# Kernel optimization log

Hardware: AMD Instinct MI355X
Metric: run time of the kernel (lower is better)

Reference implementation:

```python
import jax, jax.numpy as jnp
import numpy as np
from jax import lax

B, T, J = 32, 256, 24

def _build_adj(n):
    parent = [-1,0,0,0,1,2,3,4,5,6,7,8,9,9,9,12,13,14,16,17,18,19,20,21]
    a = np.eye(n, dtype=np.float32)
    for c in range(min(n, len(parent))):
        p = parent[c]
        if 0 <= p < n:
            a[c, p] = 1.0
            a[p, c] = 1.0
    if n > len(parent):
        for j in range(len(parent), n - 1):
            a[j, j + 1] = 1.0
            a[j + 1, j] = 1.0
    d = np.clip(a.sum(1, keepdims=True), 1.0, None)
    return jnp.asarray(a / d)

ADJ = _build_adj(J)  # [J, J] degree-normalized SMPL adjacency


def _axis_angle_to_rot6d(aa):
    # aa: [..., 3] -> [..., 6] (first two columns of rotation matrix, row-major)
    angle = jnp.linalg.norm(aa, axis=-1)
    axis = aa / (angle[..., None] + 1e-8)
    x, y, z = axis[..., 0], axis[..., 1], axis[..., 2]
    zeros = jnp.zeros_like(x)
    K = jnp.stack([zeros, -z, y, z, zeros, -x, -y, x, zeros], axis=-1)
    K = K.reshape(axis.shape[:-1] + (3, 3))
    eye = jnp.eye(3, dtype=aa.dtype)
    cos = jnp.cos(angle)[..., None, None]
    sin = jnp.sin(angle)[..., None, None]
    outer = axis[..., :, None] * axis[..., None, :]
    rot = cos * eye + (1.0 - cos) * outer + sin * K
    return rot[..., :2].reshape(aa.shape[:-1] + (6,))


def _bn(x, p, eps=1e-5):
    # inference BatchNorm2d; p = stacked [gamma, beta, mean, var], each [C]
    g, b, m, v = p
    s = g / jnp.sqrt(v + eps)
    return x * s[None, :, None, None] + (b - m * s)[None, :, None, None]


def _block(x, gcn_w, gcn_b, bn1, tcn_w, tcn_b, bn2, res_w=None, res_b=None):
    # 1x1 conv (pointwise channel mix)
    y = jnp.einsum('oc,bctj->botj', gcn_w, x) + gcn_b[None, :, None, None]
    # graph aggregation over joints
    y = jnp.einsum('bctj,jk->bctk', y, ADJ)
    y = jax.nn.relu(_bn(y, bn1))
    # temporal conv (3,1), padding (1,0); dropout is identity at inference
    y = lax.conv_general_dilated(y, tcn_w, (1, 1), ((1, 1), (0, 0)),
                                 dimension_numbers=('NCHW', 'OIHW', 'NCHW'))
    y = _bn(y + tcn_b[None, :, None, None], bn2)
    if res_w is None:
        r = x
    else:
        r = jnp.einsum('oc,bctj->botj', res_w, x) + res_b[None, :, None, None]
    return jax.nn.relu(y + r)


def setup_inputs() -> dict:
    key = jax.random.key(0)
    ks = iter(jax.random.split(key, 64))
    def rn(shape, s=0.05):
        return jax.random.normal(next(ks), shape, jnp.float32) * s
    def bnp(c):
        g = jax.random.uniform(next(ks), (c,), jnp.float32) * 0.5 + 0.75
        b = rn((c,), 0.1)
        m = rn((c,), 0.1)
        v = jax.random.uniform(next(ks), (c,), jnp.float32) * 0.5 + 0.5
        return jnp.stack([g, b, m, v])
    return {
        'x': jax.random.normal(next(ks), (B, T, J, 3), jnp.float32),
        'b1_gcn_w': rn((128, 6)), 'b1_gcn_b': rn((128,)), 'b1_bn1': bnp(128),
        'b1_tcn_w': rn((128, 128, 3, 1)), 'b1_tcn_b': rn((128,)), 'b1_bn2': bnp(128),
        'b1_res_w': rn((128, 6)), 'b1_res_b': rn((128,)),
        'b2_gcn_w': rn((128, 128)), 'b2_gcn_b': rn((128,)), 'b2_bn1': bnp(128),
        'b2_tcn_w': rn((128, 128, 3, 1)), 'b2_tcn_b': rn((128,)), 'b2_bn2': bnp(128),
        'b3_gcn_w': rn((256, 128)), 'b3_gcn_b': rn((256,)), 'b3_bn1': bnp(256),
        'b3_tcn_w': rn((256, 256, 3, 1)), 'b3_tcn_b': rn((256,)), 'b3_bn2': bnp(256),
        'b3_res_w': rn((256, 128)), 'b3_res_b': rn((256,)),
        'out_w': rn((512, 256)), 'out_b': rn((512,)),
    }


def reference(x, b1_gcn_w, b1_gcn_b, b1_bn1, b1_tcn_w, b1_tcn_b, b1_bn2, b1_res_w, b1_res_b,
              b2_gcn_w, b2_gcn_b, b2_bn1, b2_tcn_w, b2_tcn_b, b2_bn2,
              b3_gcn_w, b3_gcn_b, b3_bn1, b3_tcn_w, b3_tcn_b, b3_bn2, b3_res_w, b3_res_b,
              out_w, out_b):
    rot6d = _axis_angle_to_rot6d(x)                 # [B,T,J,6]
    f = jnp.transpose(rot6d, (0, 3, 1, 2))          # [B,6,T,J]
    f = _block(f, b1_gcn_w, b1_gcn_b, b1_bn1, b1_tcn_w, b1_tcn_b, b1_bn2, b1_res_w, b1_res_b)
    f = _block(f, b2_gcn_w, b2_gcn_b, b2_bn1, b2_tcn_w, b2_tcn_b, b2_bn2)
    f = _block(f, b3_gcn_w, b3_gcn_b, b3_bn1, b3_tcn_w, b3_tcn_b, b3_bn2, b3_res_w, b3_res_b)
    pooled = f.mean(axis=(2, 3))                    # [B,256]
    mu = pooled @ out_w.T + out_b                   # [B,512]
    return mu
```

## Files before the change

kernel.cpp:

```cpp
#include <hip/hip_runtime.h>
#include <math.h>

#define J_ 24
#define T_ 256
#define B_ 32

typedef short short8v __attribute__((ext_vector_type(8)));
typedef float f32x4  __attribute__((ext_vector_type(4)));

__device__ __forceinline__ short f2bf(float f) {
    unsigned u = __float_as_uint(f);
    u += 0x7fffu + ((u >> 16) & 1u);
    return (short)(u >> 16);
}
__device__ __forceinline__ float bf2f(short s) {
    return __uint_as_float(((unsigned)(unsigned short)s) << 16);
}

__device__ __forceinline__ void gload_lds16(const void* gsrc, void* ldst) {
    __builtin_amdgcn_global_load_lds(
        (const __attribute__((address_space(1))) void*)gsrc,
        (__attribute__((address_space(3))) void*)ldst, 16, 0, 0);
}

__device__ __constant__ int d_parent[24] = {-1,0,0,0,1,2,3,4,5,6,7,8,9,9,9,12,13,14,16,17,18,19,20,21};

__global__ void adj_init_kernel(float* __restrict__ adj_out, short* __restrict__ amix) {
    __shared__ float s_adj[576];
    const int tid = threadIdx.x;
    for (int i = tid; i < 576; i += 256) {
        const int j = i / 24, k = i % 24;
        float a = (j == k || d_parent[k] == j || d_parent[j] == k) ? 1.f : 0.f;
        float d = 0.f;
        for (int kk = 0; kk < 24; ++kk)
            d += (j == kk || d_parent[kk] == j || d_parent[j] == kk) ? 1.f : 0.f;
        const float v = a / fmaxf(d, 1.f);
        s_adj[i] = v;
        adj_out[i] = v;
    }
    __syncthreads();
    if (tid < 24) {
        float cs = 0.f;
        for (int j = 0; j < 24; ++j) cs += s_adj[j*24 + tid];
        adj_out[576 + tid] = cs;
        int n = 0;
        for (int j = 0; j < 24; ++j) {
            const float w = s_adj[j*24 + tid];
            if (w != 0.f && n < 8) {
                adj_out[600 + tid*8 + n] = w;
                adj_out[792 + tid*8 + n] = (float)j;
                ++n;
            }
        }
        for (; n < 8; ++n) { adj_out[600 + tid*8 + n] = 0.f; adj_out[792 + tid*8 + n] = 0.f; }
    }
    __syncthreads();
    for (int i = tid; i < 96*96; i += 256) {
        const int r = i / 96, j = i % 96;
        float v = 0.f;
        if (r / 24 == j / 24) v = s_adj[(j % 24) * 24 + (r % 24)];
        amix[i] = f2bf(v);
    }
}

__global__ __launch_bounds__(256) void prep_kernel(
    const float* __restrict__ w1t, const float* __restrict__ bn1_2,
    const float* __restrict__ w2t, const float* __restrict__ bn2_2,
    const float* __restrict__ w3t, const float* __restrict__ bn3_2,
    const float* __restrict__ g2w, const float* __restrict__ bn2_1,
    const float* __restrict__ g3w, const float* __restrict__ bn3_1,
    const float* __restrict__ r3w,
    const float* __restrict__ g1w, const float* __restrict__ bn1_1,
    const float* __restrict__ r1w,
    short* __restrict__ wt1b, short* __restrict__ wt2b, short* __restrict__ wt3b,
    short* __restrict__ gw2b, short* __restrict__ gw3b, short* __restrict__ rw3b,
    short* __restrict__ gw1b, short* __restrict__ rw1b)
{
    const int i = blockIdx.x * 256 + threadIdx.x;
    if (i < 49152) {
        const int o = i / 384, r = i % 384, dt = r / 128, c = r % 128;
        const float s = bn1_2[o] * rsqrtf(bn1_2[384 + o] + 1e-5f);
        wt1b[i] = f2bf(s * w1t[(o*128 + c)*3 + dt]);
    } else if (i < 98304) {
        const int j = i - 49152;
        const int o = j / 384, r = j % 384, dt = r / 128, c = r % 128;
        const float s = bn2_2[o] * rsqrtf(bn2_2[384 + o] + 1e-5f);
        wt2b[j] = f2bf(s * w2t[(o*128 + c)*3 + dt]);
    } else if (i < 294912) {
        const int j = i - 98304;
        const int o = j / 768, r = j % 768, dt = r / 256, c = r % 256;
        const float s = bn3_2[o] * rsqrtf(bn3_2[768 + o] + 1e-5f);
        wt3b[j] = f2bf(s * w3t[(o*256 + c)*3 + dt]);
    } else if (i < 311296) {
        const int j = i - 294912;
        const int o = j / 128;
        const float s = bn2_1[o] * rsqrtf(bn2_1[384 + o] + 1e-5f);
        gw2b[j] = f2bf(s * g2w[j]);
    } else if (i < 344064) {
        const int j = i - 311296;
        const int o = j / 128;
        const float s = bn3_1[o] * rsqrtf(bn3_1[768 + o] + 1e-5f);
        gw3b[j] = f2bf(s * g3w[j]);
    } else if (i < 376832) {
        const int j = i - 344064;
        rw3b[j] = f2bf(r3w[j]);
    } else if (i < 378880) {
        const int j = i - 376832;
        const int o = j / 8, c = j & 7;
        const float s = bn1_1[o] * rsqrtf(bn1_1[384 + o] + 1e-5f);
        gw1b[j] = (c < 6) ? f2bf(s * g1w[o*6 + c]) : (short)0;
    } else if (i < 380928) {
        const int j = i - 378880;
        const int o = j / 8, c = j & 7;
        rw1b[j] = (c < 6) ? f2bf(r1w[o*6 + c]) : (short)0;
    }
}

#define LDS_SZ   52832
#define FA_OFF   26624
#define FT_STRIDE 208
#define X6B_OFF  40320
#define XA6B_OFF 44928
#define TBL_OFF  51200

__global__ __launch_bounds__(512) void block1_kernel(
    const float* __restrict__ x,
    const short* __restrict__ gw1b, const float* __restrict__ gb1, const float* __restrict__ bn1,
    const short* __restrict__ rw1b, const float* __restrict__ rb1,
    const float* __restrict__ bn12, const float* __restrict__ tb1, const short* __restrict__ wt1b,
    const short* __restrict__ gw2b, const float* __restrict__ gb2, const float* __restrict__ bn21,
    const float* __restrict__ adjp, const short* __restrict__ amix,
    short* __restrict__ f1_out, short* __restrict__ h2_out)
{
    __shared__ char smem[LDS_SZ];
    short* s_x6b  = (short*)(smem + X6B_OFF);
    short* s_xa6b = (short*)(smem + XA6B_OFF);
    float* s_cw  = (float*)(smem + TBL_OFF);
    int*   s_ci  = (int*)  (smem + TBL_OFF + 768);
    float* s_cs  = (float*)(smem + TBL_OFF + 1536);

    const int r0 = blockIdx.x * 96;
    const int bstart = (r0 / 6144) * 6144;
    const int bend = bstart + 6144;
    const int tid = threadIdx.x;
    const int l = tid & 63, wid = tid >> 6;
    const int m0w = (wid >> 2) * 48;
    const int n0w = (wid & 3) * 32;
    const int lr = l & 15, lk = l >> 4;
    const short8v z8 = {0,0,0,0,0,0,0,0};

    if (tid < 192) { s_cw[tid] = adjp[600 + tid]; s_ci[tid] = (int)adjp[792 + tid]; }
    else if (tid < 216) s_cs[tid - 192] = adjp[576 + (tid - 192)];
    if (tid < 144) {
        const int gr = r0 - 24 + tid;
        short8v v = z8;
        if (gr >= bstart && gr < bend) {
            const float ax = x[gr*3+0], ay = x[gr*3+1], az = x[gr*3+2];
            const float angle = sqrtf(ax*ax + ay*ay + az*az);
            const float inv = 1.f / (angle + 1e-8f);
            const float ux = ax*inv, uy = ay*inv, uz = az*inv;
            const float c = cosf(angle), s = sinf(angle), omc = 1.f - c;
            v[0] = f2bf(c + omc*ux*ux);   v[1] = f2bf(omc*ux*uy - s*uz);
            v[2] = f2bf(omc*uy*ux + s*uz); v[3] = f2bf(c + omc*uy*uy);
            v[4] = f2bf(omc*uz*ux - s*uy); v[5] = f2bf(omc*uz*uy + s*ux);
        }
        *(short8v*)(s_x6b + tid*8) = v;
    }
    __syncthreads();
    if (tid < 144) {
        const int k = tid % 24, sl = (tid / 24) * 24;
        float a[6] = {0,0,0,0,0,0};
        #pragma unroll
        for (int u = 0; u < 8; ++u) {
            const float wgt = s_cw[k*8+u];
            const short8v v = *(const short8v*)(s_x6b + (sl + s_ci[k*8+u])*8);
            #pragma unroll
            for (int e = 0; e < 6; ++e) a[e] = fmaf(wgt, bf2f(v[e]), a[e]);
        }
        short8v o8 = z8;
        #pragma unroll
        for (int e = 0; e < 6; ++e) o8[e] = f2bf(a[e]);
        *(short8v*)(s_xa6b + tid*8) = o8;
    }
    __syncthreads();
    {
        const int col = wid*16 + lr;
        short8v bfr = z8;
        if (lk == 0) bfr = *(const short8v*)(gw1b + (size_t)col*8);
        f32x4 cacc[9];
        #pragma unroll
        for (int mi = 0; mi < 9; ++mi) cacc[mi] = (f32x4){0.f,0.f,0.f,0.f};
        #pragma unroll
        for (int mi = 0; mi < 9; ++mi) {
            short8v afr = z8;
            if (lk == 0) afr = *(const short8v*)(s_xa6b + (mi*16 + lr)*8);
            cacc[mi] = __builtin_amdgcn_mfma_f32_16x16x32_bf16(afr, bfr, cacc[mi], 0, 0, 0);
        }
        const float s1 = bn1[col] * rsqrtf(bn1[384 + col] + 1e-5f);
        const float t1 = bn1[128 + col] - bn1[256 + col] * s1;
        const float g1 = s1 * gb1[col];
        const int ch2 = col * 2;
        #pragma unroll
        for (int mi = 0; mi < 9; ++mi)
            #pragma unroll
            for (int rg = 0; rg < 4; ++rg) {
                const int row = mi*16 + lk*4 + rg;
                const int gr = r0 - 24 + row;
                short hv = 0;
                if (gr >= bstart && gr < bend)
                    hv = f2bf(fmaxf(cacc[mi][rg] + t1 + g1*s_cs[row % 24], 0.f));
                *(short*)(smem + row*256 + ((ch2 & 0xF0) ^ ((row&7)<<4)) + (ch2 & 14)) = hv;
            }
    }
    __syncthreads();
    f32x4 acc[3][2];
    #pragma unroll
    for (int mi = 0; mi < 3; ++mi)
        #pragma unroll
        for (int ni = 0; ni < 2; ++ni) acc[mi][ni] = (f32x4){0.f,0.f,0.f,0.f};
    #pragma unroll
    for (int dt = 0; dt < 3; ++dt) {
        #pragma unroll
        for (int kc = 0; kc < 4; ++kc) {
            short8v bfr[2], afr[3];
            #pragma unroll
            for (int ni = 0; ni < 2; ++ni) {
                const int n = n0w + ni*16 + lr;
                bfr[ni] = *(const short8v*)(wt1b + (size_t)n*384 + dt*128 + kc*32 + lk*8);
            }
            #pragma unroll
            for (int mi = 0; mi < 3; ++mi) {
                const int row = m0w + dt*24 + mi*16 + lr;
                afr[mi] = *(const short8v*)(smem + row*256 + ((kc*64 + lk*16) ^ ((row&7)<<4)));
            }
            #pragma unroll
            for (int mi = 0; mi < 3; ++mi)
                #pragma unroll
                for (int ni = 0; ni < 2; ++ni)
                    acc[mi][ni] = __builtin_amdgcn_mfma_f32_16x16x32_bf16(afr[mi], bfr[ni], acc[mi][ni], 0, 0, 0);
        }
    }
    {
        short8v bfr[2], afr[3];
        #pragma unroll
        for (int ni = 0; ni < 2; ++ni) {
            bfr[ni] = z8;
            if (lk == 0) bfr[ni] = *(const short8v*)(rw1b + (size_t)(n0w + ni*16 + lr)*8);
        }
        #pragma unroll
        for (int mi = 0; mi < 3; ++mi) {
            afr[mi] = z8;
            if (lk == 0) afr[mi] = *(const short8v*)(s_x6b + (m0w + mi*16 + lr + 24)*8);
        }
        #pragma unroll
        for (int mi = 0; mi < 3; ++mi)
            #pragma unroll
            for (int ni = 0; ni < 2; ++ni)
                acc[mi][ni] = __builtin_amdgcn_mfma_f32_16x16x32_bf16(afr[mi], bfr[ni], acc[mi][ni], 0, 0, 0);
    }
    __syncthreads();
    #pragma unroll
    for (int ni = 0; ni < 2; ++ni) {
        const int o = n0w + ni*16 + lr;
        const float s2 = bn12[o] * rsqrtf(bn12[384 + o] + 1e-5f);
        const float bias = (bn12[128 + o] - bn12[256 + o]*s2) + s2*tb1[o] + rb1[o];
        #pragma unroll
        for (int mi = 0; mi < 3; ++mi)
            #pragma unroll
            for (int rg = 0; rg < 4; ++rg) {
                const int rl = m0w + mi*16 + lk*4 + rg;
                const short hv = f2bf(fmaxf(acc[mi][ni][rg] + bias, 0.f));
                f1_out[(size_t)(r0 + rl)*128 + o] = hv;
                *(short*)(smem + o*FT_STRIDE + rl*2) = hv;
            }
    }
    __syncthreads();
    {
        f32x4 pacc[3][2];
        #pragma unroll
        for (int mi = 0; mi < 3; ++mi)
            #pragma unroll
            for (int ni = 0; ni < 2; ++ni) pacc[mi][ni] = (f32x4){0.f,0.f,0.f,0.f};
        #pragma unroll
        for (int kc = 0; kc < 3; ++kc) {
            short8v bfr[2], afr[3];
            #pragma unroll
            for (int ni = 0; ni < 2; ++ni) {
                const int ch = n0w + ni*16 + lr;
                bfr[ni] = *(const short8v*)(smem + ch*FT_STRIDE + kc*64 + lk*16);
            }
            #pragma unroll
            for (int mi = 0; mi < 3; ++mi) {
                const int row = m0w + mi*16 + lr;
                afr[mi] = *(const short8v*)(amix + row*96 + kc*32 + lk*8);
            }
            #pragma unroll
            for (int mi = 0; mi < 3; ++mi)
                #pragma unroll
                for (int ni = 0; ni < 2; ++ni)
                    pacc[mi][ni] = __builtin_amdgcn_mfma_f32_16x16x32_bf16(afr[mi], bfr[ni], pacc[mi][ni], 0, 0, 0);
        }
        __syncthreads();
        #pragma unroll
        for (int ni = 0; ni < 2; ++ni) {
            const int ch2 = (n0w + ni*16 + lr) * 2;
            #pragma unroll
            for (int mi = 0; mi < 3; ++mi)
                #pragma unroll
                for (int rg = 0; rg < 4; ++rg) {
                    const int row = m0w + mi*16 + lk*4 + rg;
                    *(short*)(smem + FA_OFF + row*256 + ((ch2 & 0xF0) ^ ((row&7)<<4)) + (ch2 & 14)) =
                        f2bf(pacc[mi][ni][rg]);
                }
        }
    }
    __syncthreads();
    #pragma unroll
    for (int mi = 0; mi < 3; ++mi)
        #pragma unroll
        for (int ni = 0; ni < 2; ++ni) acc[mi][ni] = (f32x4){0.f,0.f,0.f,0.f};
    #pragma unroll
    for (int kc = 0; kc < 4; ++kc) {
        short8v bfr[2], afr[3];
        #pragma unroll
        for (int ni = 0; ni < 2; ++ni) {
            const int n = n0w + ni*16 + lr;
            bfr[ni] = *(const short8v*)(gw2b + (size_t)n*128 + kc*32 + lk*8);
        }
        #pragma unroll
        for (int mi = 0; mi < 3; ++mi) {
            const int row = m0w + mi*16 + lr;
            afr[mi] = *(const short8v*)(smem + FA_OFF + row*256 + ((kc*64 + lk*16) ^ ((row&7)<<4)));
        }
        #pragma unroll
        for (int mi = 0; mi < 3; ++mi)
            #pragma unroll
            for (int ni = 0; ni < 2; ++ni)
                acc[mi][ni] = __builtin_amdgcn_mfma_f32_16x16x32_bf16(afr[mi], bfr[ni], acc[mi][ni], 0, 0, 0);
    }
    #pragma unroll
    for (int ni = 0; ni < 2; ++ni) {
        const int o = n0w + ni*16 + lr;
        const float s = bn21[o] * rsqrtf(bn21[384 + o] + 1e-5f);
        const float t = bn21[128 + o] - bn21[256 + o]*s;
        const float g = s * gb2[o];
        #pragma unroll
        for (int mi = 0; mi < 3; ++mi)
            #pragma unroll
            for (int rg = 0; rg < 4; ++rg) {
                const int rl = m0w + mi*16 + lk*4 + rg;
                h2_out[(size_t)(r0 + rl)*128 + o] = f2bf(fmaxf(acc[mi][ni][rg] + t + g*s_cs[rl % 24], 0.f));
            }
    }
}

__global__ __launch_bounds__(512) void block2_kernel(
    const short* __restrict__ h2, const short* __restrict__ wt2b,
    const float* __restrict__ bn22, const float* __restrict__ tb2,
    const short* __restrict__ f1,
    const short* __restrict__ gw3b, const float* __restrict__ gb3, const float* __restrict__ bn31,
    const float* __restrict__ adjp, const short* __restrict__ amix,
    const char* __restrict__ zbuf,
    short* __restrict__ f2_out, short* __restrict__ h3_out)
{
    __shared__ char smem[LDS_SZ];
    float* s_cs  = (float*)(smem + TBL_OFF + 1536);

    const int r0 = blockIdx.x * 96;
    const int bstart = (r0 / 6144) * 6144;
    const int bend = bstart + 6144;
    const int tid = threadIdx.x;
    const int l = tid & 63, wid = tid >> 6;
    const int m0w = (wid >> 2) * 48;
    const int lr = l & 15, lk = l >> 4;

    if (tid < 24) s_cs[tid] = adjp[576 + tid];
    for (int ck = wid; ck < 36; ck += 8) {
        const int row = ck*4 + (l >> 4);
        const int cg = (l & 15) ^ (row & 7);
        const int gr = r0 - 24 + row;
        const void* gsrc = (gr >= bstart && gr < bend)
            ? (const void*)(h2 + (size_t)gr*128 + cg*8)
            : (const void*)(zbuf + cg*16);
        gload_lds16(gsrc, smem + ck*1024);
    }
    __syncthreads();
    {
        const int n0w = (wid & 3) * 32;
        f32x4 acc[3][2];
        #pragma unroll
        for (int mi = 0; mi < 3; ++mi)
            #pragma unroll
            for (int ni = 0; ni < 2; ++ni) acc[mi][ni] = (f32x4){0.f,0.f,0.f,0.f};
        #pragma unroll
        for (int dt = 0; dt < 3; ++dt) {
            #pragma unroll
            for (int kc = 0; kc < 4; ++kc) {
                short8v bfr[2], afr[3];
                #pragma unroll
                for (int ni = 0; ni < 2; ++ni) {
                    const int n = n0w + ni*16 + lr;
                    bfr[ni] = *(const short8v*)(wt2b + (size_t)n*384 + dt*128 + kc*32 + lk*8);
                }
                #pragma unroll
                for (int mi = 0; mi < 3; ++mi) {
                    const int row = m0w + dt*24 + mi*16 + lr;
                    afr[mi] = *(const short8v*)(smem + row*256 + ((kc*64 + lk*16) ^ ((row&7)<<4)));
                }
                #pragma unroll
                for (int mi = 0; mi < 3; ++mi)
                    #pragma unroll
                    for (int ni = 0; ni < 2; ++ni)
                        acc[mi][ni] = __builtin_amdgcn_mfma_f32_16x16x32_bf16(afr[mi], bfr[ni], acc[mi][ni], 0, 0, 0);
            }
        }
        __syncthreads();
        #pragma unroll
        for (int ni = 0; ni < 2; ++ni) {
            const int o = n0w + ni*16 + lr;
            const float s = bn22[o] * rsqrtf(bn22[384 + o] + 1e-5f);
            const float bias = (bn22[128 + o] - bn22[256 + o]*s) + s*tb2[o];
            #pragma unroll
            for (int mi = 0; mi < 3; ++mi)
                #pragma unroll
                for (int rg = 0; rg < 4; ++rg) {
                    const int rl = m0w + mi*16 + lk*4 + rg;
                    const float res = bf2f(f1[(size_t)(r0 + rl)*128 + o]);
                    const short hv = f2bf(fmaxf(acc[mi][ni][rg] + bias + res, 0.f));
                    *(short*)(smem + o*FT_STRIDE + rl*2) = hv;
                    f2_out[(size_t)(r0 + rl)*128 + o] = hv;
                }
        }
    }
    __syncthreads();
    {
        const int n0w = (wid & 3) * 32;
        f32x4 pacc[3][2];
        #pragma unroll
        for (int mi = 0; mi < 3; ++mi)
            #pragma unroll
            for (int ni = 0; ni < 2; ++ni) pacc[mi][ni] = (f32x4){0.f,0.f,0.f,0.f};
        #pragma unroll
        for (int kc = 0; kc < 3; ++kc) {
            short8v bfr[2], afr[3];
            #pragma unroll
            for (int ni = 0; ni < 2; ++ni) {
                const int ch = n0w + ni*16 + lr;
                bfr[ni] = *(const short8v*)(smem + ch*FT_STRIDE + kc*64 + lk*16);
            }
            #pragma unroll
            for (int mi = 0; mi < 3; ++mi) {
                const int row = m0w + mi*16 + lr;
                afr[mi] = *(const short8v*)(amix + row*96 + kc*32 + lk*8);
            }
            #pragma unroll
            for (int mi = 0; mi < 3; ++mi)
                #pragma unroll
                for (int ni = 0; ni < 2; ++ni)
                    pacc[mi][ni] = __builtin_amdgcn_mfma_f32_16x16x32_bf16(afr[mi], bfr[ni], pacc[mi][ni], 0, 0, 0);
        }
        __syncthreads();
        #pragma unroll
        for (int ni = 0; ni < 2; ++ni) {
            const int ch2 = (n0w + ni*16 + lr) * 2;
            #pragma unroll
            for (int mi = 0; mi < 3; ++mi)
                #pragma unroll
                for (int rg = 0; rg < 4; ++rg) {
                    const int row = m0w + mi*16 + lk*4 + rg;
                    *(short*)(smem + FA_OFF + row*256 + ((ch2 & 0xF0) ^ ((row&7)<<4)) + (ch2 & 14)) =
                        f2bf(pacc[mi][ni][rg]);
                }
        }
    }
    __syncthreads();
    {
        const int n0w = (wid & 3) * 64;
        f32x4 acc[3][4];
        #pragma unroll
        for (int mi = 0; mi < 3; ++mi)
            #pragma unroll
            for (int ni = 0; ni < 4; ++ni) acc[mi][ni] = (f32x4){0.f,0.f,0.f,0.f};
        #pragma unroll
        for (int kc = 0; kc < 4; ++kc) {
            short8v bfr[4], afr[3];
            #pragma unroll
            for (int ni = 0; ni < 4; ++ni) {
                const int n = n0w + ni*16 + lr;
                bfr[ni] = *(const short8v*)(gw3b + (size_t)n*128 + kc*32 + lk*8);
            }
            #pragma unroll
            for (int mi = 0; mi < 3; ++mi) {
                const int row = m0w + mi*16 + lr;
                afr[mi] = *(const short8v*)(smem + FA_OFF + row*256 + ((kc*64 + lk*16) ^ ((row&7)<<4)));
            }
            #pragma unroll
            for (int mi = 0; mi < 3; ++mi)
                #pragma unroll
                for (int ni = 0; ni < 4; ++ni)
                    acc[mi][ni] = __builtin_amdgcn_mfma_f32_16x16x32_bf16(afr[mi], bfr[ni], acc[mi][ni], 0, 0, 0);
        }
        #pragma unroll
        for (int ni = 0; ni < 4; ++ni) {
            const int o = n0w + ni*16 + lr;
            const float s = bn31[o] * rsqrtf(bn31[768 + o] + 1e-5f);
            const float t = bn31[256 + o] - bn31[512 + o]*s;
            const float g = s * gb3[o];
            #pragma unroll
            for (int mi = 0; mi < 3; ++mi)
                #pragma unroll
                for (int rg = 0; rg < 4; ++rg) {
                    const int rl = m0w + mi*16 + lk*4 + rg;
                    h3_out[(size_t)(r0 + rl)*256 + o] = f2bf(fmaxf(acc[mi][ni][rg] + t + g*s_cs[rl % 24], 0.f));
                }
        }
    }
}

__global__ __launch_bounds__(512) void conv3_pool_kernel(
    const short* __restrict__ A, const short* __restrict__ Bw,
    const float* __restrict__ bn, const float* __restrict__ tb,
    const short* __restrict__ f2, const short* __restrict__ rw3b, const float* __restrict__ rb3,
    const char* __restrict__ zbuf, float* __restrict__ pooled)
{
    __shared__ char lds[240 * 256];
    const int cpx = gridDim.x >> 3;
    const int bid = blockIdx.x;
    const int tile = (bid % 8) * cpx + bid / 8;
    const int r0 = tile * 192;
    const int bb = r0 / 6144;
    const int bstart = bb * 6144, bend = bstart + 6144;
    const int tid = threadIdx.x, l = tid & 63, wid = tid >> 6;
    const int m0w = (wid >> 2) * 96;
    const int n0w = (wid & 3) * 64;
    const int lr = l & 15, lk = l >> 4;

    f32x4 acc[6][4];
    #pragma unroll
    for (int mi = 0; mi < 6; ++mi)
        #pragma unroll
        for (int ni = 0; ni < 4; ++ni) acc[mi][ni] = (f32x4){0.f,0.f,0.f,0.f};

    for (int p = 0; p < 2; ++p) {
        if (p) __syncthreads();
        for (int ck = wid; ck < 60; ck += 8) {
            const int row = ck*4 + (l >> 4);
            const int cg = (l & 15) ^ (row & 7);
            const int gr = r0 - 24 + row;
            const void* gsrc = (gr >= bstart && gr < bend)
                ? (const void*)(A + (size_t)gr*256 + p*128 + cg*8)
                : (const void*)(zbuf + cg*16);
            gload_lds16(gsrc, lds + ck*1024);
        }
        __syncthreads();
        #pragma unroll
        for (int dt = 0; dt < 3; ++dt) {
            #pragma unroll
            for (int kc = 0; kc < 4; ++kc) {
                short8v bfr[4], afr[6];
                #pragma unroll
                for (int ni = 0; ni < 4; ++ni) {
                    const int n = n0w + ni * 16 + lr;
                    bfr[ni] = *(const short8v*)(Bw + (size_t)n * 768 + dt * 256 + p * 128 + kc * 32 + lk * 8);
                }
                #pragma unroll
                for (int mi = 0; mi < 6; ++mi) {
                    const int row = m0w + dt * 24 + mi * 16 + lr;
                    afr[mi] = *(const short8v*)(lds + row * 256 + ((kc * 64 + lk * 16) ^ ((row & 7) << 4)));
                }
                #pragma unroll
                for (int mi = 0; mi < 6; ++mi)
                    #pragma unroll
                    for (int ni = 0; ni < 4; ++ni)
                        acc[mi][ni] = __builtin_amdgcn_mfma_f32_16x16x32_bf16(afr[mi], bfr[ni], acc[mi][ni], 0, 0, 0);
            }
        }
    }
    __syncthreads();
    for (int ck = wid; ck < 48; ck += 8) {
        const int row = ck*4 + (l >> 4);
        const int cg = (l & 15) ^ (row & 7);
        gload_lds16((const void*)(f2 + (size_t)(r0 + row)*128 + cg*8), lds + ck*1024);
    }
    __syncthreads();
    #pragma unroll
    for (int kc = 0; kc < 4; ++kc) {
        short8v bfr[4], afr[6];
        #pragma unroll
        for (int ni = 0; ni < 4; ++ni) {
            const int n = n0w + ni * 16 + lr;
            bfr[ni] = *(const short8v*)(rw3b + (size_t)n * 128 + kc * 32 + lk * 8);
        }
        #pragma unroll
        for (int mi = 0; mi < 6; ++mi) {
            const int row = m0w + mi * 16 + lr;
            afr[mi] = *(const short8v*)(lds + row * 256 + ((kc * 64 + lk * 16) ^ ((row & 7) << 4)));
        }
        #pragma unroll
        for (int mi = 0; mi < 6; ++mi)
            #pragma unroll
            for (int ni = 0; ni < 4; ++ni)
                acc[mi][ni] = __builtin_amdgcn_mfma_f32_16x16x32_bf16(afr[mi], bfr[ni], acc[mi][ni], 0, 0, 0);
    }

    float psum[4] = {0.f, 0.f, 0.f, 0.f};
    #pragma unroll
    for (int ni = 0; ni < 4; ++ni) {
        const int o = n0w + ni * 16 + lr;
        const float s = bn[o] * rsqrtf(bn[768 + o] + 1e-5f);
        const float t = bn[256 + o] - bn[512 + o] * s;
        const float bias = s * tb[o] + t + rb3[o];
        #pragma unroll
        for (int mi = 0; mi < 6; ++mi)
            #pragma unroll
            for (int rg = 0; rg < 4; ++rg)
                psum[ni] += fmaxf(acc[mi][ni][rg] + bias, 0.f);
    }
    #pragma unroll
    for (int ni = 0; ni < 4; ++ni) {
        float v = psum[ni];
        v += __shfl_xor(v, 16);
        v += __shfl_xor(v, 32);
        if (l < 16) atomicAdd(pooled + (size_t)bb * 256 + (n0w + ni * 16 + l), v);
    }
}

__global__ __launch_bounds__(256) void head_kernel(const float* __restrict__ pooled_sums,
    const float* __restrict__ ow, const float* __restrict__ ob, float* __restrict__ outp) {
    __shared__ float pooled[256];
    const int b = blockIdx.x, tid = threadIdx.x;
    pooled[tid] = pooled_sums[(size_t)b*256 + tid] * (1.f/6144.f);
    __syncthreads();
    for (int rep = 0; rep < 2; ++rep) {
        const int oo = rep*256 + tid;
        float a = ob[oo];
        const float4* wr = (const float4*)(ow + (size_t)oo*256);
        for (int c4 = 0; c4 < 64; ++c4) {
            const float4 w = wr[c4];
            const float4 p = *(const float4*)&pooled[c4*4];
            a += w.x*p.x + w.y*p.y + w.z*p.z + w.w*p.w;
        }
        outp[(size_t)b*512 + oo] = a;
    }
}

extern "C" void kernel_launch(void* const* d_in, const int* in_sizes, int n_in,
                              void* d_out, int out_size, void* d_ws, size_t ws_size,
                              hipStream_t stream)
{
    const float* x        = (const float*)d_in[0];
    const float* b1_gcn_w = (const float*)d_in[1];
    const float* b1_gcn_b = (const float*)d_in[2];
    const float* b1_bn1   = (const float*)d_in[3];
    const float* b1_tcn_w = (const float*)d_in[4];
    const float* b1_tcn_b = (const float*)d_in[5];
    const float* b1_bn2   = (const float*)d_in[6];
    const float* b1_res_w = (const float*)d_in[7];
    const float* b1_res_b = (const float*)d_in[8];
    const float* b2_gcn_w = (const float*)d_in[9];
    const float* b2_gcn_b = (const float*)d_in[10];
    const float* b2_bn1   = (const float*)d_in[11];
    const float* b2_tcn_w = (const float*)d_in[12];
    const float* b2_tcn_b = (const float*)d_in[13];
    const float* b2_bn2   = (const float*)d_in[14];
    const float* b3_gcn_w = (const float*)d_in[15];
    const float* b3_gcn_b = (const float*)d_in[16];
    const float* b3_bn1   = (const float*)d_in[17];
    const float* b3_tcn_w = (const float*)d_in[18];
    const float* b3_tcn_b = (const float*)d_in[19];
    const float* b3_bn2   = (const float*)d_in[20];
    const float* b3_res_w = (const float*)d_in[21];
    const float* b3_res_b = (const float*)d_in[22];
    const float* out_w    = (const float*)d_in[23];
    const float* out_b    = (const float*)d_in[24];

    char* w = (char*)d_ws;
    float* adjp = (float*)w;   w += 4096;
    short* wt1b = (short*)w;   w += 98304;
    short* wt2b = (short*)w;   w += 98304;
    short* wt3b = (short*)w;   w += 393216;
    short* gw2b = (short*)w;   w += 32768;
    short* gw3b = (short*)w;   w += 65536;
    short* rw3b = (short*)w;   w += 65536;
    short* amixb = (short*)w;  w += 18432;
    short* gw1b = (short*)w;   w += 4096;
    short* rw1b = (short*)w;   w += 4096;
    float* pooled = (float*)w; w += 32768;
    char* zbuf = w;            w += 1024;
    const size_t fixed = (size_t)(w - (char*)d_ws);

    int G = 1;
    {
        const int tiers[6] = {32, 16, 8, 4, 2, 1};
        for (int ti = 0; ti < 6; ++ti) {
            const size_t need = fixed + (size_t)tiers[ti] * 6291456ull;
            if (need <= ws_size) { G = tiers[ti]; break; }
        }
    }
    const size_t MG = (size_t)G * 6144;

    short* f1 = (short*)w;
    short* h2 = f1 + MG*128;
    short* h3 = h2 + MG*128;
    short* f2 = f1;

    hipMemsetAsync(pooled, 0, 32768 + 1024, stream);
    adj_init_kernel<<<1, 256, 0, stream>>>(adjp, amixb);
    prep_kernel<<<1488, 256, 0, stream>>>(b1_tcn_w, b1_bn2, b2_tcn_w, b2_bn2, b3_tcn_w, b3_bn2,
                                          b2_gcn_w, b2_bn1, b3_gcn_w, b3_bn1, b3_res_w,
                                          b1_gcn_w, b1_bn1, b1_res_w,
                                          wt1b, wt2b, wt3b, gw2b, gw3b, rw3b, gw1b, rw1b);

    for (int b0 = 0; b0 < B_; b0 += G) {
        block1_kernel<<<64*G, 512, 0, stream>>>(
            x + (size_t)b0*6144*3,
            gw1b, b1_gcn_b, b1_bn1, rw1b, b1_res_b,
            b1_bn2, b1_tcn_b, wt1b,
            gw2b, b2_gcn_b, b2_bn1, adjp, amixb, f1, h2);
        block2_kernel<<<64*G, 512, 0, stream>>>(
            h2, wt2b, b2_bn2, b2_tcn_b, f1,
            gw3b, b3_gcn_b, b3_bn1, adjp, amixb, zbuf, f2, h3);
        conv3_pool_kernel<<<32*G, 512, 0, stream>>>(
            h3, wt3b, b3_bn2, b3_tcn_b, f2, rw3b, b3_res_b, zbuf, pooled + (size_t)b0*256);
    }

    head_kernel<<<B_, 256, 0, stream>>>(pooled, out_w, out_b, (float*)d_out);
}
```

Measured before the change: 418.5 us.

## Halve conv3 tile rows and double-buffer the K-half loads in conv3_pool

Shrinks each conv3_pool block from 192 to 96 rows and doubles the grid, which gives more blocks for the CUs to schedule. It splits LDS into two buffers so the second K-half of the activation tile and the residual input load while MFMAs run on the first. This cuts accumulator registers and exposed load latency. The cost is that each block now reloads the same weights and halo rows over fewer output rows and issues more atomics into pooled.

```diff
diff --git a/kernel.cpp b/kernel.cpp
--- a/kernel.cpp
+++ b/kernel.cpp
@@ -523,81 +523,111 @@
     const short* __restrict__ f2, const short* __restrict__ rw3b, const float* __restrict__ rb3,
     const char* __restrict__ zbuf, float* __restrict__ pooled)
 {
-    __shared__ char lds[240 * 256];
+    __shared__ char lds[2 * 36864];
+    char* buf0 = lds;
+    char* buf1 = lds + 36864;
     const int cpx = gridDim.x >> 3;
     const int bid = blockIdx.x;
     const int tile = (bid % 8) * cpx + bid / 8;
-    const int r0 = tile * 192;
+    const int r0 = tile * 96;
     const int bb = r0 / 6144;
     const int bstart = bb * 6144, bend = bstart + 6144;
     const int tid = threadIdx.x, l = tid & 63, wid = tid >> 6;
-    const int m0w = (wid >> 2) * 96;
+    const int m0w = (wid >> 2) * 48;
     const int n0w = (wid & 3) * 64;
     const int lr = l & 15, lk = l >> 4;
 
-    f32x4 acc[6][4];
-    #pragma unroll
-    for (int mi = 0; mi < 6; ++mi)
+    f32x4 acc[3][4];
+    #pragma unroll
+    for (int mi = 0; mi < 3; ++mi)
         #pragma unroll
         for (int ni = 0; ni < 4; ++ni) acc[mi][ni] = (f32x4){0.f,0.f,0.f,0.f};
 
-    for (int p = 0; p < 2; ++p) {
-        if (p) __syncthreads();
-        for (int ck = wid; ck < 60; ck += 8) {
-            const int row = ck*4 + (l >> 4);
-            const int cg = (l & 15) ^ (row & 7);
-            const int gr = r0 - 24 + row;
-            const void* gsrc = (gr >= bstart && gr < bend)
-                ? (const void*)(A + (size_t)gr*256 + p*128 + cg*8)
-                : (const void*)(zbuf + cg*16);
-            gload_lds16(gsrc, lds + ck*1024);
-        }
-        __syncthreads();
-        #pragma unroll
-        for (int dt = 0; dt < 3; ++dt) {
-            #pragma unroll
-            for (int kc = 0; kc < 4; ++kc) {
-                short8v bfr[4], afr[6];
-                #pragma unroll
-                for (int ni = 0; ni < 4; ++ni) {
-                    const int n = n0w + ni * 16 + lr;
-                    bfr[ni] = *(const short8v*)(Bw + (size_t)n * 768 + dt * 256 + p * 128 + kc * 32 + lk * 8);
-                }
-                #pragma unroll
-                for (int mi = 0; mi < 6; ++mi) {
-                    const int row = m0w + dt * 24 + mi * 16 + lr;
-                    afr[mi] = *(const short8v*)(lds + row * 256 + ((kc * 64 + lk * 16) ^ ((row & 7) << 4)));
-                }
-                #pragma unroll
-                for (int mi = 0; mi < 6; ++mi)
-                    #pragma unroll
-                    for (int ni = 0; ni < 4; ++ni)
-                        acc[mi][ni] = __builtin_amdgcn_mfma_f32_16x16x32_bf16(afr[mi], bfr[ni], acc[mi][ni], 0, 0, 0);
-            }
-        }
-    }
-    __syncthreads();
-    for (int ck = wid; ck < 48; ck += 8) {
+    for (int ck = wid; ck < 36; ck += 8) {
         const int row = ck*4 + (l >> 4);
         const int cg = (l & 15) ^ (row & 7);
-        gload_lds16((const void*)(f2 + (size_t)(r0 + row)*128 + cg*8), lds + ck*1024);
+        const int gr = r0 - 24 + row;
+        const void* gsrc = (gr >= bstart && gr < bend)
+            ? (const void*)(A + (size_t)gr*256 + cg*8)
+            : (const void*)(zbuf + cg*16);
+        gload_lds16(gsrc, buf0 + ck*1024);
+    }
+    __syncthreads();
+    for (int ck = wid; ck < 36; ck += 8) {
+        const int row = ck*4 + (l >> 4);
+        const int cg = (l & 15) ^ (row & 7);
+        const int gr = r0 - 24 + row;
+        const void* gsrc = (gr >= bstart && gr < bend)
+            ? (const void*)(A + (size_t)gr*256 + 128 + cg*8)
+            : (const void*)(zbuf + cg*16);
+        gload_lds16(gsrc, buf1 + ck*1024);
+    }
+    #pragma unroll
+    for (int dt = 0; dt < 3; ++dt) {
+        #pragma unroll
+        for (int kc = 0; kc < 4; ++kc) {
+            short8v bfr[4], afr[3];
+            #pragma unroll
+            for (int ni = 0; ni < 4; ++ni) {
+                const int n = n0w + ni * 16 + lr;
+                bfr[ni] = *(const short8v*)(Bw + (size_t)n * 768 + dt * 256 + kc * 32 + lk * 8);
+            }
+            #pragma unroll
+            for (int mi = 0; mi < 3; ++mi) {
+                const int row = m0w + dt * 24 + mi * 16 + lr;
+                afr[mi] = *(const short8v*)(buf0 + row * 256 + ((kc * 64 + lk * 16) ^ ((row & 7) << 4)));
+            }
+            #pragma unroll
+            for (int mi = 0; mi < 3; ++mi)
+                #pragma unroll
+                for (int ni = 0; ni < 4; ++ni)
+                    acc[mi][ni] = __builtin_amdgcn_mfma_f32_16x16x32_bf16(afr[mi], bfr[ni], acc[mi][ni], 0, 0, 0);
+        }
+    }
+    __syncthreads();
+    for (int ck = wid; ck < 24; ck += 8) {
+        const int row = ck*4 + (l >> 4);
+        const int cg = (l & 15) ^ (row & 7);
+        gload_lds16((const void*)(f2 + (size_t)(r0 + row)*128 + cg*8), buf0 + ck*1024);
+    }
+    #pragma unroll
+    for (int dt = 0; dt < 3; ++dt) {
+        #pragma unroll
+        for (int kc = 0; kc < 4; ++kc) {
+            short8v bfr[4], afr[3];
+            #pragma unroll
+            for (int ni = 0; ni < 4; ++ni) {
+                const int n = n0w + ni * 16 + lr;
+                bfr[ni] = *(const short8v*)(Bw + (size_t)n * 768 + dt * 256 + 128 + kc * 32 + lk * 8);
+            }
+            #pragma unroll
+            for (int mi = 0; mi < 3; ++mi) {
+                const int row = m0w + dt * 24 + mi * 16 + lr;
+                afr[mi] = *(const short8v*)(buf1 + row * 256 + ((kc * 64 + lk * 16) ^ ((row & 7) << 4)));
+            }
+            #pragma unroll
+            for (int mi = 0; mi < 3; ++mi)
+                #pragma unroll
+                for (int ni = 0; ni < 4; ++ni)
+                    acc[mi][ni] = __builtin_amdgcn_mfma_f32_16x16x32_bf16(afr[mi], bfr[ni], acc[mi][ni], 0, 0, 0);
+        }
     }
     __syncthreads();
     #pragma unroll
     for (int kc = 0; kc < 4; ++kc) {
-        short8v bfr[4], afr[6];
+        short8v bfr[4], afr[3];
         #pragma unroll
         for (int ni = 0; ni < 4; ++ni) {
             const int n = n0w + ni * 16 + lr;
             bfr[ni] = *(const short8v*)(rw3b + (size_t)n * 128 + kc * 32 + lk * 8);
         }
         #pragma unroll
-        for (int mi = 0; mi < 6; ++mi) {
+        for (int mi = 0; mi < 3; ++mi) {
             const int row = m0w + mi * 16 + lr;
-            afr[mi] = *(const short8v*)(lds + row * 256 + ((kc * 64 + lk * 16) ^ ((row & 7) << 4)));
-        }
-        #pragma unroll
-        for (int mi = 0; mi < 6; ++mi)
+            afr[mi] = *(const short8v*)(buf0 + row * 256 + ((kc * 64 + lk * 16) ^ ((row & 7) << 4)));
+        }
+        #pragma unroll
+        for (int mi = 0; mi < 3; ++mi)
             #pragma unroll
             for (int ni = 0; ni < 4; ++ni)
                 acc[mi][ni] = __builtin_amdgcn_mfma_f32_16x16x32_bf16(afr[mi], bfr[ni], acc[mi][ni], 0, 0, 0);
@@ -611,7 +641,7 @@
         const float t = bn[256 + o] - bn[512 + o] * s;
         const float bias = s * tb[o] + t + rb3[o];
         #pragma unroll
-        for (int mi = 0; mi < 6; ++mi)
+        for (int mi = 0; mi < 3; ++mi)
             #pragma unroll
             for (int rg = 0; rg < 4; ++rg)
                 psum[ni] += fmaxf(acc[mi][ni][rg] + bias, 0.f);
@@ -720,7 +750,7 @@
         block2_kernel<<<64*G, 512, 0, stream>>>(
             h2, wt2b, b2_bn2, b2_tcn_b, f1,
             gw3b, b3_gcn_b, b3_bn1, adjp, amixb, zbuf, f2, h3);
-        conv3_pool_kernel<<<32*G, 512, 0, stream>>>(
+        conv3_pool_kernel<<<64*G, 512, 0, stream>>>(
             h3, wt3b, b3_bn2, b3_tcn_b, f2, rw3b, b3_res_b, zbuf, pooled + (size_t)b0*256);
     }
 
```

Result: slower. 496.0 us (+18.5%).
